# Performance work log

Hardware: AMD Instinct MI355X
Metric: run time of the kernel (lower is better)

The kernel has to match this reference:

```python
import jax, jax.numpy as jnp
import numpy as np

MIN_VAL = 1e-10


def integ_exp_trig(lam, theta, t, t0=None):
    # Analytic integrals of exp(lam*s)*cos(theta*s) and exp(lam*s)*sin(theta*s) on [t0, t].
    if t0 is None:
        t0 = jnp.zeros_like(t)
    exps_t = jnp.nan_to_num(jnp.exp(lam * t))
    exps_t0 = jnp.nan_to_num(jnp.exp(lam * t0))
    denom = jnp.square(lam) + jnp.square(theta)
    scale = jnp.sign(denom) / jnp.clip(denom, MIN_VAL)
    cos_t, sin_t = jnp.cos(theta * t), jnp.sin(theta * t)
    cos_t0, sin_t0 = jnp.cos(theta * t0), jnp.sin(theta * t0)
    res_cos = scale * (exps_t * (lam * cos_t + theta * sin_t)
                       - exps_t0 * (lam * cos_t0 + theta * sin_t0))
    res_sin = scale * (exps_t * (lam * sin_t - theta * cos_t)
                       - exps_t0 * (lam * sin_t0 - theta * cos_t0))
    return jnp.nan_to_num(res_cos), jnp.nan_to_num(res_sin)


def esde_predict_complex(X0, X0_var, U, times, Q, lam_real, lam_imag, V_real, V_imag):
    B, n = X0.shape
    m = n // 2
    lam = lam_real + 1j * lam_imag          # [B, m] complex
    V = V_real + 1j * V_imag                # [B, n, m] complex
    X0c = X0[:, :, None]                    # [B, n, 1]

    # Phi(0): exp(0*lam) = 1, so phi_comp = V
    Phi0 = jnp.concatenate([V.real, V.imag], axis=2)        # [B, n, n]
    Phi0_inv = jnp.nan_to_num(jnp.linalg.inv(Phi0))

    init_cond = Phi0_inv @ X0c                               # [B, n, 1]
    init_var = Phi0_inv @ X0_var @ jnp.swapaxes(Phi0_inv, -1, -2)

    # Phi(t)
    et = jnp.exp(times[:, None].astype(lam.dtype) * lam)     # [B, m] complex
    phi = V * et[:, None, :]                                 # right-mult by diag(et)
    Phi = jnp.nan_to_num(jnp.concatenate([phi.real, phi.imag], axis=2))  # [B, n, n]

    Hom = Phi @ init_cond
    Hom_var = Phi @ init_var @ jnp.swapaxes(Phi, -1, -2)
    # force positive diagonal: diag -> |diag|, off-diag unchanged
    eye = jnp.eye(n, dtype=Hom_var.dtype)
    diag_sign = jnp.sign(jnp.diagonal(Hom_var, axis1=-2, axis2=-1))  # [B, n]
    Hom_var = Hom_var * ((1.0 - eye) + eye * diag_sign[:, :, None])

    # ----- particular (control) term: block 2x2 rotation-integral times Phi0_inv @ U
    ext_u = (Phi0_inv @ U[:, :, None]).reshape(B, m, 2)      # interleaved (re, im) pairs
    cos_int, sin_int = integ_exp_trig(-lam.real, lam.imag, times[:, None])  # [B, m]
    li0 = cos_int * ext_u[..., 0] - sin_int * ext_u[..., 1]
    li1 = sin_int * ext_u[..., 0] + cos_int * ext_u[..., 1]
    lambda_int = jnp.stack([li0, li1], axis=-1).reshape(B, n, 1)
    Part = Phi @ lambda_int

    # ----- diffusion variance term
    ext_s = Phi0_inv @ Q @ jnp.swapaxes(Phi0_inv, -1, -2)    # [B, n, n]
    ls = lam[:, None, :] + lam[:, :, None]                   # lam_i + lam_j
    ls_conj = lam[:, None, :] - lam[:, :, None]              # lam_j - lam_i
    t3 = times[:, None, None]
    cos1, sin1 = integ_exp_trig(-ls.real, ls.imag, t3)       # [B, m, m]
    cos2, sin2 = integ_exp_trig(-ls.real, ls_conj.imag, t3)
    vcc = 0.5 * (cos1 + cos2)   # int cos*cos
    vsc = 0.5 * (sin1 + sin2)   # int sin*cos
    vcs = 0.5 * (sin1 - sin2)   # int cos*sin
    vss = 0.5 * (cos2 - cos1)   # int sin*sin
    E = ext_s.reshape(B, m, 2, m, 2)  # interleaved 2x2 block structure
    d11, d12 = E[:, :, 0, :, 0], E[:, :, 0, :, 1]
    d21, d22 = E[:, :, 1, :, 0], E[:, :, 1, :, 1]
    r11 = vcc * d11 - vsc * d21 - vcs * d12 + vss * d22
    r12 = vcs * d11 - vss * d21 + vcc * d12 - vsc * d22
    r21 = vsc * d11 + vcc * d21 - vss * d12 - vcs * d22
    r22 = vss * d11 + vcs * d21 + vsc * d12 + vcc * d22
    row0 = jnp.stack([r11, r12], axis=-1)   # [B, m, m, 2]
    row1 = jnp.stack([r21, r22], axis=-1)
    sig_int = jnp.stack([row0, row1], axis=2).reshape(B, n, n)
    Part_var = Phi @ sig_int @ jnp.swapaxes(Phi, -1, -2)

    return Hom + Part, Hom_var + Part_var


def setup_inputs() -> dict:
    key = jax.random.key(0)
    ks = jax.random.split(key, 9)
    B, n = 65536, 16
    m = n // 2
    X0 = jax.random.normal(ks[0], (B, n), jnp.float32)
    A = jax.random.normal(ks[1], (B, n, n), jnp.float32) * 0.1
    X0_var = A @ jnp.swapaxes(A, -1, -2) + 0.1 * jnp.eye(n, dtype=jnp.float32)
    U = jax.random.normal(ks[2], (B, n), jnp.float32)
    times = jax.random.uniform(ks[3], (B,), jnp.float32, 0.1, 2.0)
    Qa = jax.random.normal(ks[4], (B, n, n), jnp.float32) * 0.1
    Q = Qa @ jnp.swapaxes(Qa, -1, -2)
    lam_real = -jax.random.uniform(ks[5], (B, m), jnp.float32, 0.05, 1.0)
    lam_imag = jax.random.uniform(ks[6], (B, m), jnp.float32, -2.0, 2.0)
    V_real = jax.random.normal(ks[7], (B, n, m), jnp.float32)
    V_imag = jax.random.normal(ks[8], (B, n, m), jnp.float32)
    return {"X0": X0, "X0_var": X0_var, "U": U, "times": times, "Q": Q,
            "lam_real": lam_real, "lam_imag": lam_imag,
            "V_real": V_real, "V_imag": V_imag}


def reference(X0, X0_var, U, times, Q, lam_real, lam_imag, V_real, V_imag):
    return esde_predict_complex(X0, X0_var, U, times, Q,
                                lam_real, lam_imag, V_real, V_imag)
```

## Files before the change

kernel.cpp:

```cpp
#include <hip/hip_runtime.h>
#include <math.h>

#define WSYNC() do { __builtin_amdgcn_wave_barrier(); asm volatile("" ::: "memory"); } while (0)
#define LFENCE() asm volatile("" ::: "memory")

constexpr int FS = 20;

typedef float v2f __attribute__((ext_vector_type(2)));
__device__ inline v2f pkfma(v2f a, v2f b, v2f c) {
  return __builtin_elementwise_fma(a, b, c);
}

struct alignas(16) WaveMem {
  float P[16 * FS];
  float F[16 * FS];
  float W[16 * FS];
  float L1[16 * FS];
  float L4[16 * FS];
  float etr[8], eti[8], lamr[8], lami[8];
  float vx0[16], vu[16], vic[16];
};

__device__ inline float n2n(float v) {
  if (isnan(v)) return 0.0f;
  if (isinf(v)) return v > 0.f ? 3.402823466e38f : -3.402823466e38f;
  return v;
}

__device__ inline float readlane_f(float v, int l) {
  return __int_as_float(__builtin_amdgcn_readlane(__float_as_int(v), l));
}
template<int CTRL>
__device__ inline float dpp_f(float v) {
  return __int_as_float(__builtin_amdgcn_mov_dpp(__float_as_int(v), CTRL, 0xF, 0xF, true));
}

__device__ inline void load16(float out[16], const float* p) {
#pragma unroll
  for (int c = 0; c < 4; ++c) {
    float4 v = *(const float4*)(p + 4 * c);
    out[4*c+0] = v.x; out[4*c+1] = v.y; out[4*c+2] = v.z; out[4*c+3] = v.w;
  }
}

template<bool TRB>
__device__ inline void mmv(float* C, const float* A, const float* Bm,
                           int i16, int jg, bool absdiag = false)
{
  const int j0 = jg << 2;
  float aA[16];
  load16(aA, &A[i16 * FS]);
  float acc[4];
  if (TRB) {
#pragma unroll
    for (int cp = 0; cp < 2; ++cp) {
      float bB0[16], bB1[16];
      load16(bB0, &Bm[(j0 + 2*cp) * FS]);
      load16(bB1, &Bm[(j0 + 2*cp + 1) * FS]);
      v2f s = {0.f, 0.f};
#pragma unroll
      for (int k = 0; k < 16; ++k)
        s = pkfma((v2f){aA[k], aA[k]}, (v2f){bB0[k], bB1[k]}, s);
      acc[2*cp] = s.x; acc[2*cp+1] = s.y;
    }
  } else {
    v2f a01 = {0.f, 0.f}, a23 = {0.f, 0.f};
#pragma unroll
    for (int k = 0; k < 16; ++k) {
      float4 bv = *(const float4*)&Bm[k * FS + j0];
      v2f ad = {aA[k], aA[k]};
      a01 = pkfma(ad, (v2f){bv.x, bv.y}, a01);
      a23 = pkfma(ad, (v2f){bv.z, bv.w}, a23);
    }
    acc[0] = a01.x; acc[1] = a01.y; acc[2] = a23.x; acc[3] = a23.y;
  }
  if (absdiag) {
#pragma unroll
    for (int c = 0; c < 4; ++c) if (i16 == j0 + c) acc[c] = fabsf(acc[c]);
  }
  *(float4*)&C[i16 * FS + j0] = make_float4(acc[0], acc[1], acc[2], acc[3]);
}

__global__ __launch_bounds__(256, 6) void nesde_kernel(
    const float* __restrict__ gX0, const float* __restrict__ gXv,
    const float* __restrict__ gU,  const float* __restrict__ gT,
    const float* __restrict__ gQ,  const float* __restrict__ gLr,
    const float* __restrict__ gLi, const float* __restrict__ gVr,
    const float* __restrict__ gVi, float* __restrict__ gOut0,
    float* __restrict__ gOut1, int B)
{
  __shared__ WaveMem sm[4];
  const int wid  = threadIdx.x >> 6;
  const int lane = threadIdx.x & 63;
  const int b = blockIdx.x * 4 + wid;
  if (b >= B) return;
  WaveMem& S = sm[wid];

  const int r4  = lane >> 2;
  const int q   = lane & 3;
  const int i16 = lane & 15;
  const int jg  = lane >> 4;
  const int j0  = jg << 2;

  const float t = gT[b];

  const float4 xv = *(const float4*)(gXv + (size_t)b * 256 + lane * 4);
  const float4 qv = *(const float4*)(gQ  + (size_t)b * 256 + lane * 4);
  float4 v4;
  {
    const float* src = (q < 2) ? gVr : gVi;
    v4 = *(const float4*)(src + (size_t)b * 128 + r4 * 8 + ((q & 1) << 2));
  }
  float x0u = 0.f;
  if (q == 2) x0u = gX0[(size_t)b * 16 + r4];
  if (q == 3) x0u = gU [(size_t)b * 16 + r4];

  if (lane < 8) {
    float lr = gLr[(size_t)b * 8 + lane];
    float li = gLi[(size_t)b * 8 + lane];
    S.lamr[lane] = lr; S.lami[lane] = li;
    float e = expf(lr * t);
    float sn, cs; sincosf(li * t, &sn, &cs);
    S.etr[lane] = e * cs;
    S.eti[lane] = e * sn;
  }
  WSYNC();

  float4 vco;
  {
    const int p = lane >> 3, qq = lane & 7;
    float la  = -(S.lamr[p] + S.lamr[qq]);
    float th1 = S.lami[p] + S.lami[qq];
    float th2 = S.lami[qq] - S.lami[p];
    float exps = __expf(la * t);
    float s1, c1, s2, c2;
    __sincosf(th1 * t, &s1, &c1);
    __sincosf(th2 * t, &s2, &c2);
    float den1 = la * la + th1 * th1;
    float sg1 = (den1 > 0.f) ? 1.f : ((den1 < 0.f) ? -1.f : 0.f);
    float sc1 = sg1 / fmaxf(den1, 1e-10f);
    float cos1 = sc1 * (exps * (la * c1 + th1 * s1) - la);
    float sin1 = sc1 * (exps * (la * s1 - th1 * c1) + th1);
    float den2 = la * la + th2 * th2;
    float sg2 = (den2 > 0.f) ? 1.f : ((den2 < 0.f) ? -1.f : 0.f);
    float sc2 = sg2 / fmaxf(den2, 1e-10f);
    float cos2 = sc2 * (exps * (la * c2 + th2 * s2) - la);
    float sin2 = sc2 * (exps * (la * s2 - th2 * c2) + th2);
    vco = make_float4(0.5f * (cos1 + cos2), 0.5f * (sin1 + sin2),
                      0.5f * (sin1 - sin2), 0.5f * (cos2 - cos1));
  }
  {
    const int si = lane >> 2, sj = (lane & 3) * 4;
    *(float4*)&S.L1[si * FS + sj] = xv;
    *(float4*)&S.L4[si * FS + sj] = qv;
  }
  if (q == 2) S.vx0[r4] = x0u;
  if (q == 3) S.vu[r4]  = x0u;

  float mv[4] = { v4.x, v4.y, v4.z, v4.w };
  float pvv[4];
#pragma unroll
  for (int e = 0; e < 4; ++e) pvv[e] = __shfl_xor(mv[e], 2);
  {
    const int cbase = (q & 1) << 2;
    float er[4], ei[4], ph[4];
#pragma unroll
    for (int e = 0; e < 4; ++e) { er[e] = S.etr[cbase + e]; ei[e] = S.eti[cbase + e]; }
    if (q < 2) {
#pragma unroll
      for (int e = 0; e < 4; ++e) ph[e] = mv[e] * er[e] - pvv[e] * ei[e];
    } else {
#pragma unroll
      for (int e = 0; e < 4; ++e) ph[e] = pvv[e] * ei[e] + mv[e] * er[e];
    }
    *(float4*)&S.F[r4 * FS + (q << 2)] = make_float4(ph[0], ph[1], ph[2], ph[3]);
  }

  float a[4] = { mv[0], mv[1], mv[2], mv[3] };
  unsigned used = 0, plo = 0, phh = 0;
  int myk = 0;
#pragma unroll
  for (int k = 0; k < 16; ++k) {
    const int kq = k >> 2, ke = k & 3;
    float av = a[ke];
    float ck = (kq == 0) ? dpp_f<0x00>(av) : (kq == 1) ? dpp_f<0x55>(av)
             : (kq == 2) ? dpp_f<0xAA>(av) : dpp_f<0xFF>(av);
    float cand = ((used >> r4) & 1u) ? -1.0f : fabsf(ck);
    float mx = cand;
    mx = fmaxf(mx, dpp_f<0x124>(mx));
    mx = fmaxf(mx, dpp_f<0x128>(mx));
    mx = fmaxf(mx, dpp_f<0x142>(mx));
    mx = fmaxf(mx, dpp_f<0x143>(mx));
    float smx = readlane_f(mx, 63);
    unsigned long long msk = __ballot(cand == smx);
    const int pl4 = (__ffsll((long long)msk) - 1) & 60;
    const bool isp = ((lane & 60) == pl4);
    if (isp) *(float4*)&S.W[q << 2] = make_float4(a[0], a[1], a[2], a[3]);
    float pval = readlane_f(av, pl4 | kq);
    float pivinv = 1.0f / pval;
    LFENCE();
    float4 rr4 = *(const float4*)&S.W[q << 2];
    LFENCE();
    const v2f pivd = { pivinv, pivinv };
    const v2f nck  = { -ck, -ck };
    {
      v2f sp = (v2f){ rr4.x, rr4.y } * pivd;
      v2f up = pkfma(nck, sp, (v2f){ a[0], a[1] });
      a[0] = isp ? sp.x : up.x;
      a[1] = isp ? sp.y : up.y;
      v2f sp2 = (v2f){ rr4.z, rr4.w } * pivd;
      v2f up2 = pkfma(nck, sp2, (v2f){ a[2], a[3] });
      a[2] = isp ? sp2.x : up2.x;
      a[3] = isp ? sp2.y : up2.y;
    }
    if (q == kq) a[ke] = isp ? pivinv : -(ck * pivinv);
    used |= 1u << (pl4 >> 2);
    if (isp) myk = k;
    const unsigned p = (unsigned)(pl4 >> 2);
    if (k < 8) plo |= p << (4 * k); else phh |= p << (4 * (k - 8));
  }

  {
#pragma unroll
    for (int e = 0; e < 4; ++e) {
      const int c = (q << 2) + e;
      const unsigned nib = (q < 2) ? (plo >> (4 * c)) : (phh >> (4 * (c - 8)));
      S.P[myk * FS + (nib & 15u)] = n2n(a[e]);
    }
  }
  WSYNC();

  if (lane < 32) {
    const float* src = (lane < 16) ? S.vx0 : S.vu;
    float sv[16], pA[16];
    load16(pA, &S.P[i16 * FS]);
    load16(sv, src);
    float d = 0.f;
#pragma unroll
    for (int k = 0; k < 16; ++k) d = fmaf(pA[k], sv[k], d);
    if (lane < 16) S.vic[i16] = d; else S.vu[i16] = d;
  }
  WSYNC();
  if (lane < 8) {
    float la = -S.lamr[lane], th = S.lami[lane];
    float exps = expf(la * t);
    float sn, cs; sincosf(th * t, &sn, &cs);
    float denom = la * la + th * th;
    float sgn = (denom > 0.f) ? 1.f : ((denom < 0.f) ? -1.f : 0.f);
    float scale = sgn / fmaxf(denom, 1e-10f);
    float ci = scale * (exps * (la * cs + th * sn) - la);
    float si = scale * (exps * (la * sn - th * cs) + th);
    float e0 = S.vu[2 * lane], e1 = S.vu[2 * lane + 1];
    S.vic[2 * lane]     += ci * e0 - si * e1;
    S.vic[2 * lane + 1] += si * e0 + ci * e1;
  }
  WSYNC();
  if (lane < 16) {
    float fA[16], vv[16];
    load16(fA, &S.F[lane * FS]);
    load16(vv, S.vic);
    float d = 0.f;
#pragma unroll
    for (int k = 0; k < 16; ++k) d = fmaf(fA[k], vv[k], d);
    gOut0[(size_t)b * 16 + lane] = d;
  }
  WSYNC();

  mmv<true >(S.W,  S.P, S.L4, i16, jg);        WSYNC();
  mmv<true >(S.L4, S.W, S.P,  i16, jg);        WSYNC();
  mmv<false>(S.W,  S.F, S.P,  i16, jg);        WSYNC();
  mmv<true >(S.P,  S.W, S.L1, i16, jg);        WSYNC();
  mmv<true >(S.L1, S.P, S.W,  i16, jg, true);  WSYNC();

  {
    const int p2 = i16 >> 1, aa = i16 & 1;
    const int sA = p2 * 8 + (j0 >> 1);
    float4 c0, c1;
    c0.x = __shfl(vco.x, sA);     c0.y = __shfl(vco.y, sA);
    c0.z = __shfl(vco.z, sA);     c0.w = __shfl(vco.w, sA);
    c1.x = __shfl(vco.x, sA + 1); c1.y = __shfl(vco.y, sA + 1);
    c1.z = __shfl(vco.z, sA + 1); c1.w = __shfl(vco.w, sA + 1);
    float4 top = *(const float4*)&S.L4[(2 * p2) * FS + j0];
    float4 bot = *(const float4*)&S.L4[(2 * p2 + 1) * FS + j0];
    float tl[4] = { top.x, top.y, top.z, top.w };
    float bl[4] = { bot.x, bot.y, bot.z, bot.w };
    float r[4];
#pragma unroll
    for (int uu = 0; uu < 4; ++uu) {
      float4 c = (uu < 2) ? c0 : c1;
      const int off = 2 * (uu >> 1);
      float d11 = tl[off], d12 = tl[off + 1];
      float d21 = bl[off], d22 = bl[off + 1];
      const int bb = uu & 1;
      if (aa == 0)
        r[uu] = (bb == 0) ? (c.x * d11 - c.y * d21 - c.z * d12 + c.w * d22)
                          : (c.z * d11 - c.w * d21 + c.x * d12 - c.y * d22);
      else
        r[uu] = (bb == 0) ? (c.y * d11 + c.x * d21 - c.w * d12 - c.z * d22)
                          : (c.w * d11 + c.z * d21 + c.y * d12 + c.x * d22);
    }
    *(float4*)&S.W[i16 * FS + j0] = make_float4(r[0], r[1], r[2], r[3]);
  }
  WSYNC();
  mmv<false>(S.L4, S.F, S.W, i16, jg);         WSYNC();

  {
    float aA[16];
    load16(aA, &S.L4[i16 * FS]);
    float acc[4];
#pragma unroll
    for (int cp = 0; cp < 2; ++cp) {
      float bB0[16], bB1[16];
      load16(bB0, &S.F[(j0 + 2*cp) * FS]);
      load16(bB1, &S.F[(j0 + 2*cp + 1) * FS]);
      v2f s = {0.f, 0.f};
#pragma unroll
      for (int k = 0; k < 16; ++k)
        s = pkfma((v2f){aA[k], aA[k]}, (v2f){bB0[k], bB1[k]}, s);
      acc[2*cp] = s.x; acc[2*cp+1] = s.y;
    }
    float4 hv = *(const float4*)&S.L1[i16 * FS + j0];
    float4 o = make_float4(hv.x + acc[0], hv.y + acc[1], hv.z + acc[2], hv.w + acc[3]);
    *(float4*)&gOut1[(size_t)b * 256 + i16 * 16 + j0] = o;
  }
}

extern "C" void kernel_launch(void* const* d_in, const int* in_sizes, int n_in,
                              void* d_out, int out_size, void* d_ws, size_t ws_size,
                              hipStream_t stream) {
  const float* X0 = (const float*)d_in[0];
  const float* Xv = (const float*)d_in[1];
  const float* U  = (const float*)d_in[2];
  const float* T  = (const float*)d_in[3];
  const float* Q  = (const float*)d_in[4];
  const float* Lr = (const float*)d_in[5];
  const float* Li = (const float*)d_in[6];
  const float* Vr = (const float*)d_in[7];
  const float* Vi = (const float*)d_in[8];
  const int B = in_sizes[3];
  float* out0 = (float*)d_out;
  float* out1 = (float*)d_out + (size_t)B * 16;
  const int blocks = (B + 3) / 4;
  hipLaunchKernelGGL(nesde_kernel, dim3(blocks), dim3(256), 0, stream,
                     X0, Xv, U, T, Q, Lr, Li, Vr, Vi, out0, out1, B);
}
```

Before: 179.7 us.

## Compute per-wave 16x16 matrix products with FP64 MFMA instructions

Replaces the scalar packed-FMA 16x16 matrix products in the covariance chain with the 16x16x4 FP64 MFMA instruction, converting float operands to double. Each lane loads a 4-element slice, and the results are written back to shared memory transposed through the accumulator layout. The Hom_var result is now kept in accumulator registers and used to seed the final MFMA, instead of going through shared memory. This is meant to cut VALU instruction count and LDS reads, at the cost of FP64 conversions, scattered non-vector LDS and global stores, and the MFMA's lower FP64 throughput.

```diff
diff --git a/kernel.cpp b/kernel.cpp
--- a/kernel.cpp
+++ b/kernel.cpp
@@ -7,6 +7,7 @@
 constexpr int FS = 20;
 
 typedef float v2f __attribute__((ext_vector_type(2)));
+typedef double v4d __attribute__((ext_vector_type(4)));
 __device__ inline v2f pkfma(v2f a, v2f b, v2f c) {
   return __builtin_elementwise_fma(a, b, c);
 }
@@ -44,41 +45,30 @@
 }
 
 template<bool TRB>
-__device__ inline void mmv(float* C, const float* A, const float* Bm,
-                           int i16, int jg, bool absdiag = false)
+__device__ inline v4d mmfma(const float* A, const float* Bm, int lane, v4d acc)
 {
-  const int j0 = jg << 2;
-  float aA[16];
-  load16(aA, &A[i16 * FS]);
-  float acc[4];
+  const int row = lane & 15, kl = lane >> 4;
+  float4 av = *(const float4*)&A[row * FS + 4 * kl];
+  float an[4] = { av.x, av.y, av.z, av.w };
+  float bn[4];
   if (TRB) {
-#pragma unroll
-    for (int cp = 0; cp < 2; ++cp) {
-      float bB0[16], bB1[16];
-      load16(bB0, &Bm[(j0 + 2*cp) * FS]);
-      load16(bB1, &Bm[(j0 + 2*cp + 1) * FS]);
-      v2f s = {0.f, 0.f};
-#pragma unroll
-      for (int k = 0; k < 16; ++k)
-        s = pkfma((v2f){aA[k], aA[k]}, (v2f){bB0[k], bB1[k]}, s);
-      acc[2*cp] = s.x; acc[2*cp+1] = s.y;
-    }
+    float4 bv = *(const float4*)&Bm[row * FS + 4 * kl];
+    bn[0] = bv.x; bn[1] = bv.y; bn[2] = bv.z; bn[3] = bv.w;
   } else {
-    v2f a01 = {0.f, 0.f}, a23 = {0.f, 0.f};
-#pragma unroll
-    for (int k = 0; k < 16; ++k) {
-      float4 bv = *(const float4*)&Bm[k * FS + j0];
-      v2f ad = {aA[k], aA[k]};
-      a01 = pkfma(ad, (v2f){bv.x, bv.y}, a01);
-      a23 = pkfma(ad, (v2f){bv.z, bv.w}, a23);
-    }
-    acc[0] = a01.x; acc[1] = a01.y; acc[2] = a23.x; acc[3] = a23.y;
-  }
-  if (absdiag) {
-#pragma unroll
-    for (int c = 0; c < 4; ++c) if (i16 == j0 + c) acc[c] = fabsf(acc[c]);
-  }
-  *(float4*)&C[i16 * FS + j0] = make_float4(acc[0], acc[1], acc[2], acc[3]);
+#pragma unroll
+    for (int g = 0; g < 4; ++g) bn[g] = Bm[(g + 4 * kl) * FS + row];
+  }
+#pragma unroll
+  for (int g = 0; g < 4; ++g)
+    acc = __builtin_amdgcn_mfma_f64_16x16x4f64((double)an[g], (double)bn[g],
+                                               acc, 0, 0, 0);
+  return acc;
+}
+__device__ inline void mmstore(float* C, int lane, v4d acc) {
+  const int row = lane & 15, kl = lane >> 4;
+#pragma unroll
+  for (int r = 0; r < 4; ++r)
+    C[(kl + 4 * r) * FS + row] = (float)acc[r];
 }
 
 __global__ __launch_bounds__(256, 6) void nesde_kernel(
@@ -219,7 +209,6 @@
     const unsigned p = (unsigned)(pl4 >> 2);
     if (k < 8) plo |= p << (4 * k); else phh |= p << (4 * (k - 8));
   }
-
   {
 #pragma unroll
     for (int e = 0; e < 4; ++e) {
@@ -266,11 +255,18 @@
   }
   WSYNC();
 
-  mmv<true >(S.W,  S.P, S.L4, i16, jg);        WSYNC();
-  mmv<true >(S.L4, S.W, S.P,  i16, jg);        WSYNC();
-  mmv<false>(S.W,  S.F, S.P,  i16, jg);        WSYNC();
-  mmv<true >(S.P,  S.W, S.L1, i16, jg);        WSYNC();
-  mmv<true >(S.L1, S.P, S.W,  i16, jg, true);  WSYNC();
+  const v4d z4 = { 0.0, 0.0, 0.0, 0.0 };
+  mmstore(S.W,  lane, mmfma<false>(S.P, S.L4, lane, z4));  WSYNC();
+  mmstore(S.L4, lane, mmfma<true >(S.W, S.P,  lane, z4));  WSYNC();
+  mmstore(S.W,  lane, mmfma<false>(S.F, S.P,  lane, z4));  WSYNC();
+  mmstore(S.P,  lane, mmfma<false>(S.W, S.L1, lane, z4));  WSYNC();
+  v4d hv = mmfma<true>(S.P, S.W, lane, z4);
+  {
+    const int row = lane & 15, kl = lane >> 4;
+#pragma unroll
+    for (int r = 0; r < 4; ++r) if (kl + 4 * r == row) hv[r] = fabs(hv[r]);
+  }
+  WSYNC();
 
   {
     const int p2 = i16 >> 1, aa = i16 & 1;
@@ -299,29 +295,18 @@
         r[uu] = (bb == 0) ? (c.y * d11 + c.x * d21 - c.w * d12 - c.z * d22)
                           : (c.w * d11 + c.z * d21 + c.y * d12 + c.x * d22);
     }
+    LFENCE();
     *(float4*)&S.W[i16 * FS + j0] = make_float4(r[0], r[1], r[2], r[3]);
   }
   WSYNC();
-  mmv<false>(S.L4, S.F, S.W, i16, jg);         WSYNC();
-
-  {
-    float aA[16];
-    load16(aA, &S.L4[i16 * FS]);
-    float acc[4];
-#pragma unroll
-    for (int cp = 0; cp < 2; ++cp) {
-      float bB0[16], bB1[16];
-      load16(bB0, &S.F[(j0 + 2*cp) * FS]);
-      load16(bB1, &S.F[(j0 + 2*cp + 1) * FS]);
-      v2f s = {0.f, 0.f};
-#pragma unroll
-      for (int k = 0; k < 16; ++k)
-        s = pkfma((v2f){aA[k], aA[k]}, (v2f){bB0[k], bB1[k]}, s);
-      acc[2*cp] = s.x; acc[2*cp+1] = s.y;
-    }
-    float4 hv = *(const float4*)&S.L1[i16 * FS + j0];
-    float4 o = make_float4(hv.x + acc[0], hv.y + acc[1], hv.z + acc[2], hv.w + acc[3]);
-    *(float4*)&gOut1[(size_t)b * 256 + i16 * 16 + j0] = o;
+  mmstore(S.L4, lane, mmfma<false>(S.F, S.W, lane, z4));   WSYNC();
+
+  {
+    v4d o = mmfma<true>(S.L4, S.F, lane, hv);
+    const int row = lane & 15, kl = lane >> 4;
+#pragma unroll
+    for (int r = 0; r < 4; ++r)
+      gOut1[(size_t)b * 256 + (kl + 4 * r) * 16 + row] = (float)o[r];
   }
 }
 
```

New measurement: 184.2 us. 1.02x slower.
